# Kernel optimization log

Hardware: AMD Instinct MI355X
Metric: run time of the kernel (lower is better)

Reference implementation:

```python
import jax, jax.numpy as jnp
import numpy as np

N_NODES = 100000
N_EDGES = 1600000
IN_CH = 256
HID_CH = 128


def setup_inputs() -> dict:
    key = jax.random.key(0)
    k1, k2, k3 = jax.random.split(key, 3)
    x = jax.random.normal(k1, (N_NODES, IN_CH), dtype=jnp.float32)
    edge_index = jax.random.randint(k2, (2, N_EDGES), 0, N_NODES, dtype=jnp.int64)
    # Glorot-style init for the GCN linear weight [in, out]
    W = jax.random.normal(k3, (IN_CH, HID_CH), dtype=jnp.float32) / np.sqrt(IN_CH)
    bias = jnp.zeros((HID_CH,), dtype=jnp.float32)
    # PReLU default init 0.25, per-channel
    alpha = jnp.full((HID_CH,), 0.25, dtype=jnp.float32)
    return {"x": x, "edge_index": edge_index, "W": W, "bias": bias, "alpha": alpha}


def reference(x, edge_index, W, bias, alpha):
    # GCNConv (PyG defaults): add self loops, symmetric degree norm,
    # linear transform then scatter-add aggregation, then per-channel PReLU.
    N = x.shape[0]
    self_loops = jnp.arange(N, dtype=edge_index.dtype)
    row = jnp.concatenate([edge_index[0], self_loops])  # source j
    col = jnp.concatenate([edge_index[1], self_loops])  # target i
    # degree of destination nodes (edge_weight = 1)
    deg = jax.ops.segment_sum(jnp.ones_like(col, dtype=x.dtype), col, num_segments=N)
    dinv = jnp.where(deg > 0, jax.lax.rsqrt(deg), jnp.zeros_like(deg))
    norm = dinv[row] * dinv[col]  # [E+N]
    h = x @ W  # [N, hid] dense transform first (GCNConv order)
    msgs = h[row] * norm[:, None]  # gather + scale, [E+N, hid]
    agg = jax.ops.segment_sum(msgs, col, num_segments=N) + bias  # scatter-add
    # PReLU with per-channel alpha
    return jnp.where(agg > 0, agg, alpha * agg)
```

## Files before the change

### kernel.cpp

```cpp
#include <hip/hip_runtime.h>

#define N_NODES 100000
#define N_EDGES 1600000
#define IN_CH 256
#define HID_CH 128
#define SCAN_BLOCKS ((N_NODES + 255) / 256)

typedef __attribute__((ext_vector_type(8))) short short8;
typedef __attribute__((ext_vector_type(4))) float floatx4;

static __device__ __forceinline__ unsigned short f2bf(float f) {
    unsigned int u = __float_as_uint(f);
    u += 0x7fffu + ((u >> 16) & 1u);
    return (unsigned short)(u >> 16);
}

static __device__ __forceinline__ unsigned cvt_pk_bf16(float lo, float hi) {
    unsigned r;
    asm("v_cvt_pk_bf16_f32 %0, %1, %2" : "=v"(r) : "v"(lo), "v"(hi));
    return r;
}


__global__ void count_kernel(const int* __restrict__ dst, int* __restrict__ counts,
                             int* __restrict__ rank) {
    int e = blockIdx.x * blockDim.x + threadIdx.x;
    if (e < N_EDGES) rank[e] = atomicAdd(&counts[dst[e]], 1);
}

__global__ void scanA_kernel(const int* __restrict__ counts, int* __restrict__ row_start,
                             int* __restrict__ partials) {
    __shared__ int ss[256];
    int tid = threadIdx.x;
    int i = blockIdx.x * 256 + tid;
    int v = (i < N_NODES) ? counts[i] : 0;
    ss[tid] = v;
    __syncthreads();
    for (int off = 1; off < 256; off <<= 1) {
        int t = (tid >= off) ? ss[tid - off] : 0;
        __syncthreads();
        ss[tid] += t;
        __syncthreads();
    }
    if (i < N_NODES) row_start[i] = ss[tid] - v;
    if (tid == 255) partials[blockIdx.x] = ss[255];
}

__global__ void scanB_kernel(int* __restrict__ partials) {
    __shared__ int ss[512];
    int tid = threadIdx.x;
    int v = (tid < SCAN_BLOCKS) ? partials[tid] : 0;
    ss[tid] = v;
    __syncthreads();
    for (int off = 1; off < 512; off <<= 1) {
        int t = (tid >= off) ? ss[tid - off] : 0;
        __syncthreads();
        ss[tid] += t;
        __syncthreads();
    }
    if (tid < SCAN_BLOCKS) partials[tid] = ss[tid] - v;
}

__global__ void scanC_kernel(int* __restrict__ row_start, const int* __restrict__ partials,
                             const int* __restrict__ counts, float* __restrict__ dinv) {
    int i = blockIdx.x * 256 + threadIdx.x;
    if (i >= N_NODES) return;
    row_start[i] += partials[blockIdx.x];
    dinv[i] = rsqrtf((float)(counts[i] + 1));
    if (i == 0) row_start[N_NODES] = N_EDGES;
}

__global__ void reorder_kernel(const int* __restrict__ ei, const int* __restrict__ rank,
                               const int* __restrict__ row_start, int* __restrict__ sorted) {
    int e = blockIdx.x * blockDim.x + threadIdx.x;
    if (e >= N_EDGES) return;
    int dst = ei[N_EDGES + e];
    sorted[row_start[dst] + rank[e]] = ei[e];
}


__global__ void wt_kernel(const float* __restrict__ W, unsigned short* __restrict__ Wt) {
    int i = blockIdx.x * blockDim.x + threadIdx.x;
    if (i >= IN_CH * HID_CH) return;
    int k = i >> 7;
    int c = i & 127;
    Wt[c * IN_CH + k] = f2bf(W[i]);
}


__launch_bounds__(512)
__global__ void gemm_mfma_kernel(const float* __restrict__ x,
                                 const unsigned short* __restrict__ Wt,
                                 const float* __restrict__ dinv,
                                 unsigned short* __restrict__ hp) {
    __shared__ unsigned short Bs[IN_CH * HID_CH];

    int tid = threadIdx.x;

    {
        const uint4* src = (const uint4*)Wt;
#pragma unroll
        for (int i = 0; i < 8; ++i) {
            int j = i * 512 + tid;
            unsigned lb = (unsigned)j * 16u;
            unsigned c7 = (lb >> 9) & 7u;
            unsigned db = lb ^ (c7 << 4);
            *(uint4*)((char*)Bs + db) = src[j];
        }
    }
    __syncthreads();

    int wave = tid >> 6;
    int lane = tid & 63;
    int row0 = blockIdx.x * 256 + wave * 32;
    if (row0 >= N_NODES) return;

    int m = lane & 15;
    int q = lane >> 4;

    floatx4 acc[2][8];
#pragma unroll
    for (int i = 0; i < 2; ++i)
#pragma unroll
        for (int t = 0; t < 8; ++t) acc[i][t] = (floatx4){0.f, 0.f, 0.f, 0.f};

    const float* xp0 = &x[(size_t)(row0 + m) * IN_CH + q * 8];
    const float* xp1 = xp0 + 16 * IN_CH;

    float4 aA[4], aB[4];

#define LOADA(buf, kstep)                                          \
    do {                                                           \
        const float* p0_ = xp0 + (kstep) * 32;                     \
        const float* p1_ = xp1 + (kstep) * 32;                     \
        buf[0] = *(const float4*)(p0_);                            \
        buf[1] = *(const float4*)(p0_ + 4);                        \
        buf[2] = *(const float4*)(p1_);                            \
        buf[3] = *(const float4*)(p1_ + 4);                        \
    } while (0)

#define COMPUTE(buf, kstep)                                                     \
    do {                                                                        \
        union { short8 v; unsigned u[4]; } af0_, af1_;                          \
        af0_.u[0] = cvt_pk_bf16(buf[0].x, buf[0].y);                            \
        af0_.u[1] = cvt_pk_bf16(buf[0].z, buf[0].w);                            \
        af0_.u[2] = cvt_pk_bf16(buf[1].x, buf[1].y);                            \
        af0_.u[3] = cvt_pk_bf16(buf[1].z, buf[1].w);                            \
        af1_.u[0] = cvt_pk_bf16(buf[2].x, buf[2].y);                            \
        af1_.u[1] = cvt_pk_bf16(buf[2].z, buf[2].w);                            \
        af1_.u[2] = cvt_pk_bf16(buf[3].x, buf[3].y);                            \
        af1_.u[3] = cvt_pk_bf16(buf[3].z, buf[3].w);                            \
        int kb_ = ((kstep) * 32 + q * 8) * 2;                                   \
        _Pragma("unroll")                                                       \
        for (int t = 0; t < 8; ++t) {                                           \
            int c_ = t * 16 + m;                                                \
            unsigned db_ = (unsigned)(c_ * 512 + kb_) ^ ((unsigned)(c_ & 7) << 4); \
            short8 bf_ = *(const short8*)((const char*)Bs + db_);               \
            acc[0][t] = __builtin_amdgcn_mfma_f32_16x16x32_bf16(af0_.v, bf_, acc[0][t], 0, 0, 0); \
            acc[1][t] = __builtin_amdgcn_mfma_f32_16x16x32_bf16(af1_.v, bf_, acc[1][t], 0, 0, 0); \
        }                                                                       \
    } while (0)

    LOADA(aA, 0);
#pragma unroll 1
    for (int ks = 0; ks < 8; ks += 2) {
        LOADA(aB, ks + 1);
        COMPUTE(aA, ks);
        if (ks < 6) LOADA(aA, ks + 2);
        COMPUTE(aB, ks + 1);
    }

#undef LOADA
#undef COMPUTE

#pragma unroll
    for (int tile = 0; tile < 2; ++tile) {
#pragma unroll
        for (int reg = 0; reg < 4; ++reg) {
            int grow = row0 + tile * 16 + q * 4 + reg;
            float di = dinv[grow];
            unsigned short* op = &hp[(size_t)grow * HID_CH + m];
#pragma unroll
            for (int tp = 0; tp < 4; ++tp) {
                unsigned d = cvt_pk_bf16(acc[tile][2 * tp][reg] * di,
                                         acc[tile][2 * tp + 1][reg] * di);
                op[(2 * tp) * 16]     = (unsigned short)(d & 0xffffu);
                op[(2 * tp + 1) * 16] = (unsigned short)(d >> 16);
            }
        }
    }
}


static __device__ __forceinline__ void acc_bf16x8(float* acc, uint4 u, float w) {
    acc[0] += w * __uint_as_float(u.x << 16);
    acc[1] += w * __uint_as_float(u.x & 0xffff0000u);
    acc[2] += w * __uint_as_float(u.y << 16);
    acc[3] += w * __uint_as_float(u.y & 0xffff0000u);
    acc[4] += w * __uint_as_float(u.z << 16);
    acc[5] += w * __uint_as_float(u.z & 0xffff0000u);
    acc[6] += w * __uint_as_float(u.w << 16);
    acc[7] += w * __uint_as_float(u.w & 0xffff0000u);
}

__launch_bounds__(256)
__global__ void gather_finalize_kernel(const int* __restrict__ row_start,
                                       const int* __restrict__ sorted,
                                       const float* __restrict__ dinv,
                                       const unsigned short* __restrict__ hp,
                                       const float* __restrict__ bias,
                                       const float* __restrict__ alpha,
                                       float* __restrict__ out) {
    int node = (blockIdx.x * blockDim.x + threadIdx.x) >> 6;
    int lane = threadIdx.x & 63;
    if (node >= N_NODES) return;

    int beg = row_start[node];
    int end = row_start[node + 1];
    int part = lane >> 4;
    int ch = (lane & 15) * 8;

    float di = dinv[node];
    uint4 us = *(const uint4*)&hp[(size_t)node * HID_CH + ch];

    float acc[8];
#pragma unroll
    for (int i = 0; i < 8; ++i) acc[i] = 0.f;

    for (int k = beg + part; k < end; k += 16) {
        int k1 = k + 4, k2 = k + 8, k3 = k + 12;
        int e1 = end - 1;
        int s0 = sorted[k];
        int s1 = sorted[k1 < end ? k1 : e1];
        int s2 = sorted[k2 < end ? k2 : e1];
        int s3 = sorted[k3 < end ? k3 : e1];
        uint4 u0 = *(const uint4*)&hp[(size_t)s0 * HID_CH + ch];
        uint4 u1 = *(const uint4*)&hp[(size_t)s1 * HID_CH + ch];
        uint4 u2 = *(const uint4*)&hp[(size_t)s2 * HID_CH + ch];
        uint4 u3 = *(const uint4*)&hp[(size_t)s3 * HID_CH + ch];
        float w1 = k1 < end ? 1.f : 0.f;
        float w2 = k2 < end ? 1.f : 0.f;
        float w3 = k3 < end ? 1.f : 0.f;
        acc_bf16x8(acc, u0, 1.f);
        acc_bf16x8(acc, u1, w1);
        acc_bf16x8(acc, u2, w2);
        acc_bf16x8(acc, u3, w3);
    }

#pragma unroll
    for (int i = 0; i < 8; ++i) {
        acc[i] += __shfl_xor(acc[i], 16);
        acc[i] += __shfl_xor(acc[i], 32);
    }

    if (part == 0) {
        float sf[8];
        sf[0] = __uint_as_float(us.x << 16);
        sf[1] = __uint_as_float(us.x & 0xffff0000u);
        sf[2] = __uint_as_float(us.y << 16);
        sf[3] = __uint_as_float(us.y & 0xffff0000u);
        sf[4] = __uint_as_float(us.z << 16);
        sf[5] = __uint_as_float(us.z & 0xffff0000u);
        sf[6] = __uint_as_float(us.w << 16);
        sf[7] = __uint_as_float(us.w & 0xffff0000u);

        float4 b0 = *(const float4*)&bias[ch];
        float4 b1 = *(const float4*)&bias[ch + 4];
        float4 a0 = *(const float4*)&alpha[ch];
        float4 a1 = *(const float4*)&alpha[ch + 4];
        float bv[8] = {b0.x, b0.y, b0.z, b0.w, b1.x, b1.y, b1.z, b1.w};
        float av[8] = {a0.x, a0.y, a0.z, a0.w, a1.x, a1.y, a1.z, a1.w};

        float r[8];
#pragma unroll
        for (int i = 0; i < 8; ++i) {
            float v = di * (acc[i] + sf[i]) + bv[i];
            r[i] = v > 0.f ? v : av[i] * v;
        }
        float4 o0 = make_float4(r[0], r[1], r[2], r[3]);
        float4 o1 = make_float4(r[4], r[5], r[6], r[7]);
        *(float4*)&out[(size_t)node * HID_CH + ch] = o0;
        *(float4*)&out[(size_t)node * HID_CH + ch + 4] = o1;
    }
}


extern "C" void kernel_launch(void* const* d_in, const int* in_sizes, int n_in,
                              void* d_out, int out_size, void* d_ws, size_t ws_size,
                              hipStream_t stream) {
    const float* x     = (const float*)d_in[0];
    const int*   ei    = (const int*)d_in[1];
    const float* W     = (const float*)d_in[2];
    const float* bias  = (const float*)d_in[3];
    const float* alpha = (const float*)d_in[4];
    float* out = (float*)d_out;

    char* p = (char*)d_ws;
    auto align512 = [](size_t v) { return (v + 511) / 512 * 512; };
    unsigned short* hp = (unsigned short*)p; p += align512((size_t)N_NODES * HID_CH * 2);
    unsigned short* Wt = (unsigned short*)p; p += align512((size_t)IN_CH * HID_CH * 2);
    int* counts    = (int*)p;   p += align512((size_t)N_NODES * 4);
    float* dinv    = (float*)p; p += align512((size_t)N_NODES * 4);
    int* row_start = (int*)p;   p += align512((size_t)(N_NODES + 1) * 4);
    int* rank      = (int*)p;   p += align512((size_t)N_EDGES * 4);
    int* partials  = (int*)p;   p += align512(512 * 4);
    int* sorted    = (int*)p;   p += align512((size_t)N_EDGES * 4);

    hipMemsetAsync(counts, 0, (size_t)N_NODES * sizeof(int), stream);

    count_kernel<<<(N_EDGES + 255) / 256, 256, 0, stream>>>(ei + N_EDGES, counts, rank);
    scanA_kernel<<<SCAN_BLOCKS, 256, 0, stream>>>(counts, row_start, partials);
    scanB_kernel<<<1, 512, 0, stream>>>(partials);
    scanC_kernel<<<SCAN_BLOCKS, 256, 0, stream>>>(row_start, partials, counts, dinv);
    reorder_kernel<<<(N_EDGES + 255) / 256, 256, 0, stream>>>(ei, rank, row_start, sorted);

    wt_kernel<<<(IN_CH * HID_CH + 255) / 256, 256, 0, stream>>>(W, Wt);

    gemm_mfma_kernel<<<(N_NODES + 255) / 256, 512, 0, stream>>>(x, Wt, dinv, hp);

    long long gthreads = (long long)N_NODES * 64;
    gather_finalize_kernel<<<(int)((gthreads + 255) / 256), 256, 0, stream>>>(
        row_start, sorted, dinv, hp, bias, alpha, out);
}
```

Measured before the change: 356.5 us.

## Replace global-atomic CSR build with two-pass LDS bucketed counting sort

```diff
diff --git a/kernel.cpp b/kernel.cpp
--- a/kernel.cpp
+++ b/kernel.cpp
@@ -4,7 +4,12 @@
 #define N_EDGES 1600000
 #define IN_CH 256
 #define HID_CH 128
-#define SCAN_BLOCKS ((N_NODES + 255) / 256)
+
+#define NBUCK 196
+#define NBLKC 400
+#define EPB   4000
+#define SCAN2_LEN (NBUCK * NBLKC)
+#define SCAN2_BLOCKS ((SCAN2_LEN + 255) / 256)
 
 typedef __attribute__((ext_vector_type(8))) short short8;
 typedef __attribute__((ext_vector_type(4))) float floatx4;
@@ -22,18 +27,23 @@
 }
 
 
-__global__ void count_kernel(const int* __restrict__ dst, int* __restrict__ counts,
-                             int* __restrict__ rank) {
-    int e = blockIdx.x * blockDim.x + threadIdx.x;
-    if (e < N_EDGES) rank[e] = atomicAdd(&counts[dst[e]], 1);
-}
-
-__global__ void scanA_kernel(const int* __restrict__ counts, int* __restrict__ row_start,
-                             int* __restrict__ partials) {
+__global__ void hist_kernel(const int* __restrict__ dst, int* __restrict__ histT) {
+    __shared__ int h[NBUCK];
+    int tid = threadIdx.x, blk = blockIdx.x;
+    for (int b = tid; b < NBUCK; b += 256) h[b] = 0;
+    __syncthreads();
+    int base = blk * EPB;
+    for (int e = base + tid; e < base + EPB; e += 256)
+        atomicAdd(&h[dst[e] >> 9], 1);
+    __syncthreads();
+    for (int b = tid; b < NBUCK; b += 256) histT[b * NBLKC + blk] = h[b];
+}
+
+__global__ void gscanA_kernel(int* __restrict__ data, int* __restrict__ partials) {
     __shared__ int ss[256];
     int tid = threadIdx.x;
     int i = blockIdx.x * 256 + tid;
-    int v = (i < N_NODES) ? counts[i] : 0;
+    int v = (i < SCAN2_LEN) ? data[i] : 0;
     ss[tid] = v;
     __syncthreads();
     for (int off = 1; off < 256; off <<= 1) {
@@ -42,14 +52,14 @@
         ss[tid] += t;
         __syncthreads();
     }
-    if (i < N_NODES) row_start[i] = ss[tid] - v;
+    if (i < SCAN2_LEN) data[i] = ss[tid] - v;
     if (tid == 255) partials[blockIdx.x] = ss[255];
 }
 
-__global__ void scanB_kernel(int* __restrict__ partials) {
+__global__ void gscanB_kernel(int* __restrict__ partials) {
     __shared__ int ss[512];
     int tid = threadIdx.x;
-    int v = (tid < SCAN_BLOCKS) ? partials[tid] : 0;
+    int v = (tid < SCAN2_BLOCKS) ? partials[tid] : 0;
     ss[tid] = v;
     __syncthreads();
     for (int off = 1; off < 512; off <<= 1) {
@@ -58,24 +68,70 @@
         ss[tid] += t;
         __syncthreads();
     }
-    if (tid < SCAN_BLOCKS) partials[tid] = ss[tid] - v;
-}
-
-__global__ void scanC_kernel(int* __restrict__ row_start, const int* __restrict__ partials,
-                             const int* __restrict__ counts, float* __restrict__ dinv) {
+    if (tid < SCAN2_BLOCKS) partials[tid] = ss[tid] - v;
+}
+
+__global__ void gscanC_kernel(int* __restrict__ data, const int* __restrict__ partials) {
     int i = blockIdx.x * 256 + threadIdx.x;
-    if (i >= N_NODES) return;
-    row_start[i] += partials[blockIdx.x];
-    dinv[i] = rsqrtf((float)(counts[i] + 1));
-    if (i == 0) row_start[N_NODES] = N_EDGES;
-}
-
-__global__ void reorder_kernel(const int* __restrict__ ei, const int* __restrict__ rank,
-                               const int* __restrict__ row_start, int* __restrict__ sorted) {
-    int e = blockIdx.x * blockDim.x + threadIdx.x;
-    if (e >= N_EDGES) return;
-    int dst = ei[N_EDGES + e];
-    sorted[row_start[dst] + rank[e]] = ei[e];
+    if (i < SCAN2_LEN) data[i] += partials[blockIdx.x];
+}
+
+__global__ void scatter_coarse_kernel(const int* __restrict__ ei,
+                                      const int* __restrict__ offs,
+                                      unsigned* __restrict__ bucketed) {
+    __shared__ int cur[NBUCK];
+    int tid = threadIdx.x, blk = blockIdx.x;
+    for (int b = tid; b < NBUCK; b += 256) cur[b] = offs[b * NBLKC + blk];
+    __syncthreads();
+    int base = blk * EPB;
+    for (int e = base + tid; e < base + EPB; e += 256) {
+        int src = ei[e];
+        int dst = ei[N_EDGES + e];
+        int b = dst >> 9;
+        int pos = atomicAdd(&cur[b], 1);
+        bucketed[pos] = ((unsigned)src << 9) | (unsigned)(dst & 511);
+    }
+}
+
+__global__ void fine_kernel(const unsigned* __restrict__ bucketed,
+                            const int* __restrict__ offs,
+                            int* __restrict__ sorted,
+                            int* __restrict__ row_start,
+                            float* __restrict__ dinv) {
+    __shared__ int bins[512];
+    __shared__ int scanbuf[512];
+    int b = blockIdx.x, tid = threadIdx.x;
+    int bs = offs[b * NBLKC];
+    int be = (b < NBUCK - 1) ? offs[(b + 1) * NBLKC] : N_EDGES;
+
+    bins[tid] = 0;
+    __syncthreads();
+    for (int k = bs + tid; k < be; k += 512)
+        atomicAdd(&bins[bucketed[k] & 511u], 1);
+    __syncthreads();
+
+    int c = bins[tid];
+    scanbuf[tid] = c;
+    __syncthreads();
+    for (int off = 1; off < 512; off <<= 1) {
+        int t = (tid >= off) ? scanbuf[tid - off] : 0;
+        __syncthreads();
+        scanbuf[tid] += t;
+        __syncthreads();
+    }
+    int excl = scanbuf[tid] - c;
+
+    int node = b * 512 + tid;
+    if (node <= N_NODES) row_start[node] = bs + excl;
+    if (node < N_NODES) dinv[node] = rsqrtf((float)(c + 1));
+
+    bins[tid] = bs + excl;
+    __syncthreads();
+    for (int k = bs + tid; k < be; k += 512) {
+        unsigned p = bucketed[k];
+        int pos = atomicAdd(&bins[p & 511u], 1);
+        sorted[pos] = (int)(p >> 9);
+    }
 }
 
 
@@ -124,8 +180,10 @@
 #pragma unroll
         for (int t = 0; t < 8; ++t) acc[i][t] = (floatx4){0.f, 0.f, 0.f, 0.f};
 
-    const float* xp0 = &x[(size_t)(row0 + m) * IN_CH + q * 8];
-    const float* xp1 = xp0 + 16 * IN_CH;
+    int r0 = row0 + m;        if (r0 >= N_NODES) r0 = N_NODES - 1;
+    int r1 = row0 + 16 + m;   if (r1 >= N_NODES) r1 = N_NODES - 1;
+    const float* xp0 = &x[(size_t)r0 * IN_CH + q * 8];
+    const float* xp1 = &x[(size_t)r1 * IN_CH + q * 8];
 
     float4 aA[4], aB[4];
 
@@ -178,14 +236,16 @@
 #pragma unroll
         for (int reg = 0; reg < 4; ++reg) {
             int grow = row0 + tile * 16 + q * 4 + reg;
-            float di = dinv[grow];
-            unsigned short* op = &hp[(size_t)grow * HID_CH + m];
-#pragma unroll
-            for (int tp = 0; tp < 4; ++tp) {
-                unsigned d = cvt_pk_bf16(acc[tile][2 * tp][reg] * di,
-                                         acc[tile][2 * tp + 1][reg] * di);
-                op[(2 * tp) * 16]     = (unsigned short)(d & 0xffffu);
-                op[(2 * tp + 1) * 16] = (unsigned short)(d >> 16);
+            if (grow < N_NODES) {
+                float di = dinv[grow];
+                unsigned short* op = &hp[(size_t)grow * HID_CH + m];
+#pragma unroll
+                for (int tp = 0; tp < 4; ++tp) {
+                    unsigned d = cvt_pk_bf16(acc[tile][2 * tp][reg] * di,
+                                             acc[tile][2 * tp + 1][reg] * di);
+                    op[(2 * tp) * 16]     = (unsigned short)(d & 0xffffu);
+                    op[(2 * tp + 1) * 16] = (unsigned short)(d >> 16);
+                }
             }
         }
     }
@@ -299,20 +359,19 @@
     auto align512 = [](size_t v) { return (v + 511) / 512 * 512; };
     unsigned short* hp = (unsigned short*)p; p += align512((size_t)N_NODES * HID_CH * 2);
     unsigned short* Wt = (unsigned short*)p; p += align512((size_t)IN_CH * HID_CH * 2);
-    int* counts    = (int*)p;   p += align512((size_t)N_NODES * 4);
     float* dinv    = (float*)p; p += align512((size_t)N_NODES * 4);
     int* row_start = (int*)p;   p += align512((size_t)(N_NODES + 1) * 4);
-    int* rank      = (int*)p;   p += align512((size_t)N_EDGES * 4);
+    int* histT     = (int*)p;   p += align512((size_t)SCAN2_LEN * 4);
     int* partials  = (int*)p;   p += align512(512 * 4);
+    unsigned* bucketed = (unsigned*)p; p += align512((size_t)N_EDGES * 4);
     int* sorted    = (int*)p;   p += align512((size_t)N_EDGES * 4);
 
-    hipMemsetAsync(counts, 0, (size_t)N_NODES * sizeof(int), stream);
-
-    count_kernel<<<(N_EDGES + 255) / 256, 256, 0, stream>>>(ei + N_EDGES, counts, rank);
-    scanA_kernel<<<SCAN_BLOCKS, 256, 0, stream>>>(counts, row_start, partials);
-    scanB_kernel<<<1, 512, 0, stream>>>(partials);
-    scanC_kernel<<<SCAN_BLOCKS, 256, 0, stream>>>(row_start, partials, counts, dinv);
-    reorder_kernel<<<(N_EDGES + 255) / 256, 256, 0, stream>>>(ei, rank, row_start, sorted);
+    hist_kernel<<<NBLKC, 256, 0, stream>>>(ei + N_EDGES, histT);
+    gscanA_kernel<<<SCAN2_BLOCKS, 256, 0, stream>>>(histT, partials);
+    gscanB_kernel<<<1, 512, 0, stream>>>(partials);
+    gscanC_kernel<<<SCAN2_BLOCKS, 256, 0, stream>>>(histT, partials);
+    scatter_coarse_kernel<<<NBLKC, 256, 0, stream>>>(ei, histT, bucketed);
+    fine_kernel<<<NBUCK, 512, 0, stream>>>(bucketed, histT, sorted, row_start, dinv);
 
     wt_kernel<<<(IN_CH * HID_CH + 255) / 256, 256, 0, stream>>>(W, Wt);
 
```

New measurement: 296.6 us. -16.8%, faster.
